# Optimization experiments

Measured on AMD Instinct MI355X. Metric: run time of the kernel, lower is better.

Reference implementation:

```python
import jax, jax.numpy as jnp
import numpy as np

B, N, D, M = 8, 8192, 256, 2  # M from init_kwargs


def setup_inputs() -> dict:
    key = jax.random.key(0)
    ks = jax.random.split(key, 10)
    g_names = ['G_l_ii', 'G_l_ij', 'G_l_ji', 'G_l_jj', 'G_u_ii', 'G_u_ij', 'G_u_ji', 'G_u_jj']
    inp = {'input': jax.random.normal(ks[0], (B, N, D), dtype=jnp.float32)}
    for i, name in enumerate(g_names):
        inp[name] = jax.random.normal(ks[1 + i], (B, N - 1), dtype=jnp.float32)
    inp['Diag'] = jax.random.normal(ks[9], (B, N), dtype=jnp.float32)
    inp['transform'] = 1
    return inp


def _banded_sweep(x, a0, b0, lo, dm, hi, aL, bL):
    # One tridiagonal Givens sweep over axis 1 of x [B,N,D].
    # row 0:       a0*x[0]   + b0*x[1]
    # rows 1..N-2: lo*x[i-1] + dm*x[i] + hi*x[i+1]
    # row N-1:     aL*x[N-2] + bL*x[N-1]
    n = x.shape[1]
    y0 = a0[:, None, None] * x[:, 0:1] + b0[:, None, None] * x[:, 1:2]
    ym = (lo[:, :, None] * x[:, :-2]
          + dm[:, :, None] * x[:, 1:n - 1]
          + hi[:, :, None] * x[:, 2:])
    yl = aL[:, None, None] * x[:, n - 2:n - 1] + bL[:, None, None] * x[:, n - 1:n]
    return jnp.concatenate([y0, ym, yl], axis=1)


def _forward(x, gl_ii, gl_ij, gl_ji, gl_jj, gu_ii, gu_ij, gu_ji, gu_jj, diag, transform):
    b, n, d = x.shape
    if transform:
        # stride permutation (only defined for even N in the original)
        x = x.reshape(b, n // M, M, d).transpose(0, 2, 1, 3).reshape(b, n, d)
    else:
        x = diag[:, :, None] * x
    # upper sweep -> Y
    y = _banded_sweep(
        x,
        gu_ii[:, 0], gu_ij[:, 0],
        gu_ji[:, :-1], gu_jj[:, :-1] * gu_ii[:, 1:], gu_jj[:, :-1] * gu_ij[:, 1:],
        gu_ji[:, n - 2], gu_jj[:, n - 2])
    # lower sweep -> Z
    z = _banded_sweep(
        y,
        gl_ii[:, 0], gl_ij[:, 0],
        gl_ii[:, 1:] * gl_ji[:, :-1], gl_ii[:, 1:] * gl_jj[:, :-1], gl_ij[:, 1:],
        gl_ji[:, n - 2], gl_jj[:, n - 2])
    if transform:
        z = diag[:, :, None] * z
    else:
        z = z.reshape(b, n // M, M, d).transpose(0, 2, 1, 3).reshape(b, n, d)
    return z


def reference(input, G_l_ii, G_l_ij, G_l_ji, G_l_jj, G_u_ii, G_u_ij, G_u_ji, G_u_jj, Diag, transform):
    return _forward(input, G_l_ii, G_l_ij, G_l_ji, G_l_jj,
                    G_u_ii, G_u_ij, G_u_ji, G_u_jj, Diag, transform)
```

## Files before the change

### kernel.cpp

```cpp
#include <hip/hip_runtime.h>

#define NN 8192
#define DD 256
#define NH (NN / 2)
#define BB 8
#define RPW 8
#define WPB 4
#define NBLK (BB * NN / RPW / WPB)
#define CPX (NBLK / 8)

typedef float fx4 __attribute__((ext_vector_type(4)));

__device__ __forceinline__ float4 gload4(const float* p) {
    fx4 t;
    asm volatile("global_load_dwordx4 %0, %1, off" : "=v"(t) : "v"(p) : "memory");
    return make_float4(t.x, t.y, t.z, t.w);
}

__device__ __forceinline__ float4 f4_scale(float s, float4 v) {
    return make_float4(s * v.x, s * v.y, s * v.z, s * v.w);
}
__device__ __forceinline__ float4 f4_fma(float s, float4 v, float4 a) {
    return make_float4(fmaf(s, v.x, a.x), fmaf(s, v.y, a.y),
                       fmaf(s, v.z, a.z), fmaf(s, v.w, a.w));
}

__global__ __launch_bounds__(256) void dhhp_kernel(
    const float* __restrict__ x,
    const float* __restrict__ gl_ii, const float* __restrict__ gl_ij,
    const float* __restrict__ gl_ji, const float* __restrict__ gl_jj,
    const float* __restrict__ gu_ii, const float* __restrict__ gu_ij,
    const float* __restrict__ gu_ji, const float* __restrict__ gu_jj,
    const float* __restrict__ diag, const int* __restrict__ transform,
    float* __restrict__ out)
{
    const int bid = blockIdx.x;
    const int swz = (bid & 7) * CPX + (bid >> 3);
    int wid = swz * WPB + (threadIdx.x >> 6);
    wid = __builtin_amdgcn_readfirstlane(wid);
    const int b   = wid >> 10;
    const int j0  = (wid & 1023) << 3;
    const int col = (threadIdx.x & 63) << 2;
    const int tr  = *transform;

    const float* xb  = x    + (size_t)b * NN * DD;
    const float* db  = diag + (size_t)b * NN;
    const float* uii = gu_ii + (size_t)b * (NN - 1);
    const float* uij = gu_ij + (size_t)b * (NN - 1);
    const float* uji = gu_ji + (size_t)b * (NN - 1);
    const float* ujj = gu_jj + (size_t)b * (NN - 1);
    const float* lii = gl_ii + (size_t)b * (NN - 1);
    const float* lij = gl_ij + (size_t)b * (NN - 1);
    const float* lji = gl_ji + (size_t)b * (NN - 1);
    const float* ljj = gl_jj + (size_t)b * (NN - 1);
    float* ob = out + (size_t)b * NN * DD;

    int ics[RPW + 4];
    const float* ap[RPW + 4];
    #pragma unroll
    for (int t = 0; t < RPW + 4; ++t) {
        int i  = j0 - 2 + t;
        int ic = i < 0 ? 0 : (i > NN - 1 ? NN - 1 : i);
        ics[t] = ic;
        int r  = tr ? ((ic < NH) ? (ic << 1) : (((ic - NH) << 1) | 1)) : ic;
        ap[t]  = xb + (size_t)r * DD + col;
    }
    float4 xr[RPW + 4];
    #pragma unroll
    for (int t = 0; t < RPW + 4; ++t) xr[t] = gload4(ap[t]);
    asm volatile("s_waitcnt vmcnt(0)" ::: "memory");

    if (!tr) {
        #pragma unroll
        for (int t = 0; t < RPW + 4; ++t) xr[t] = f4_scale(db[ics[t]], xr[t]);
    }

    auto yInner = [&](int i, float4 xm, float4 xc, float4 xp) -> float4 {
        float lo  = uji[i - 1];
        float cjj = ujj[i - 1];
        float dm  = cjj * uii[i];
        float hi  = cjj * uij[i];
        float4 r = f4_scale(lo, xm);
        r = f4_fma(dm, xc, r);
        r = f4_fma(hi, xp, r);
        return r;
    };
    auto yAny = [&](int i, float4 xm, float4 xc, float4 xp) -> float4 {
        int ic = i < 0 ? 0 : (i > NN - 1 ? NN - 1 : i);
        if (ic == 0)      return f4_fma(uii[0], xc, f4_scale(uij[0], xp));
        if (ic == NN - 1) return f4_fma(uji[NN - 2], xm, f4_scale(ujj[NN - 2], xc));
        return yInner(ic, xm, xc, xp);
    };
    auto zInner = [&](int j, float4 ym, float4 yc, float4 yp) -> float4 {
        float ci = lii[j];
        float lo = ci * lji[j - 1];
        float dm = ci * ljj[j - 1];
        float hi = lij[j];
        float4 r = f4_scale(lo, ym);
        r = f4_fma(dm, yc, r);
        r = f4_fma(hi, yp, r);
        return r;
    };
    auto zAny = [&](int j, float4 ym, float4 yc, float4 yp) -> float4 {
        if (j == 0)      return f4_fma(lii[0], yc, f4_scale(lij[0], yp));
        if (j == NN - 1) return f4_fma(lji[NN - 2], ym, f4_scale(ljj[NN - 2], yc));
        return zInner(j, ym, yc, yp);
    };
    auto storeRow = [&](int j, float4 z) {
        int jo;
        float4 o;
        if (tr) { o = f4_scale(db[j], z); jo = j; }
        else    { o = z; jo = (j & 1) ? (NH + (j >> 1)) : (j >> 1); }
        *reinterpret_cast<float4*>(ob + (size_t)jo * DD + col) = o;
    };

    float4 yr[RPW + 2];
    const bool interior = (j0 >= 2) && (j0 <= NN - RPW - 2);

    if (interior) {
        #pragma unroll
        for (int t = 0; t < RPW + 2; ++t)
            yr[t] = yInner(j0 - 1 + t, xr[t], xr[t + 1], xr[t + 2]);
        #pragma unroll
        for (int t = 0; t < RPW; ++t)
            storeRow(j0 + t, zInner(j0 + t, yr[t], yr[t + 1], yr[t + 2]));
    } else {
        #pragma unroll
        for (int t = 0; t < RPW + 2; ++t)
            yr[t] = yAny(j0 - 1 + t, xr[t], xr[t + 1], xr[t + 2]);
        #pragma unroll
        for (int t = 0; t < RPW; ++t)
            storeRow(j0 + t, zAny(j0 + t, yr[t], yr[t + 1], yr[t + 2]));
    }
}

extern "C" void kernel_launch(void* const* d_in, const int* in_sizes, int n_in,
                              void* d_out, int out_size, void* d_ws, size_t ws_size,
                              hipStream_t stream) {
    const float* x     = (const float*)d_in[0];
    const float* gl_ii = (const float*)d_in[1];
    const float* gl_ij = (const float*)d_in[2];
    const float* gl_ji = (const float*)d_in[3];
    const float* gl_jj = (const float*)d_in[4];
    const float* gu_ii = (const float*)d_in[5];
    const float* gu_ij = (const float*)d_in[6];
    const float* gu_ji = (const float*)d_in[7];
    const float* gu_jj = (const float*)d_in[8];
    const float* diag  = (const float*)d_in[9];
    const int* transform = (const int*)d_in[10];
    float* out = (float*)d_out;

    dim3 grid(NBLK);
    dim3 block(256);
    hipLaunchKernelGGL(dhhp_kernel, grid, block, 0, stream,
                       x, gl_ii, gl_ij, gl_ji, gl_jj,
                       gu_ii, gu_ij, gu_ji, gu_jj, diag, transform, out);
}
```

Before: 30.83 us.

## Process two row tiles per wave with staged vmcnt waits to overlap loads

Each wave now handles two 8-row tiles instead of one, so the grid is halved. All 24 row loads for both tiles are issued up front. Partial s_waitcnt vmcnt waits then let the first tile's compute and stores run while the second tile's loads are still in flight. This aims to raise memory-level parallelism per wave and hide load latency, at the cost of more registers and hand-counted vmcnt values that depend on the order loads and stores complete.

```diff
diff --git a/kernel.cpp b/kernel.cpp
--- a/kernel.cpp
+++ b/kernel.cpp
@@ -6,8 +6,11 @@
 #define BB 8
 #define RPW 8
 #define WPB 4
-#define NBLK (BB * NN / RPW / WPB)
+#define RPT (RPW * WPB)
+#define TPB 2
+#define NBLK (BB * NN / (RPT * TPB))
 #define CPX (NBLK / 8)
+#define WROWS (RPW + 4)
 
 typedef float fx4 __attribute__((ext_vector_type(4)));
 
@@ -36,10 +39,9 @@
 {
     const int bid = blockIdx.x;
     const int swz = (bid & 7) * CPX + (bid >> 3);
-    int wid = swz * WPB + (threadIdx.x >> 6);
-    wid = __builtin_amdgcn_readfirstlane(wid);
-    const int b   = wid >> 10;
-    const int j0  = (wid & 1023) << 3;
+    const int b   = __builtin_amdgcn_readfirstlane(swz >> 7);
+    const int t0  = __builtin_amdgcn_readfirstlane((swz & 127) << 6);
+    const int w   = __builtin_amdgcn_readfirstlane(threadIdx.x >> 6);
     const int col = (threadIdx.x & 63) << 2;
     const int tr  = *transform;
 
@@ -55,25 +57,31 @@
     const float* ljj = gl_jj + (size_t)b * (NN - 1);
     float* ob = out + (size_t)b * NN * DD;
 
-    int ics[RPW + 4];
-    const float* ap[RPW + 4];
+    const int j0a = t0 + (w << 3);
+    const int j0b = j0a + RPT;
+
+    int icsA[WROWS], icsB[WROWS];
+    const float* apA[WROWS];
+    const float* apB[WROWS];
     #pragma unroll
-    for (int t = 0; t < RPW + 4; ++t) {
-        int i  = j0 - 2 + t;
-        int ic = i < 0 ? 0 : (i > NN - 1 ? NN - 1 : i);
-        ics[t] = ic;
-        int r  = tr ? ((ic < NH) ? (ic << 1) : (((ic - NH) << 1) | 1)) : ic;
-        ap[t]  = xb + (size_t)r * DD + col;
+    for (int t = 0; t < WROWS; ++t) {
+        int ia  = j0a - 2 + t;
+        int ica = ia < 0 ? 0 : (ia > NN - 1 ? NN - 1 : ia);
+        icsA[t] = ica;
+        int ra  = tr ? ((ica < NH) ? (ica << 1) : (((ica - NH) << 1) | 1)) : ica;
+        apA[t]  = xb + (size_t)ra * DD + col;
+        int ib  = j0b - 2 + t;
+        int icb = ib < 0 ? 0 : (ib > NN - 1 ? NN - 1 : ib);
+        icsB[t] = icb;
+        int rb  = tr ? ((icb < NH) ? (icb << 1) : (((icb - NH) << 1) | 1)) : icb;
+        apB[t]  = xb + (size_t)rb * DD + col;
     }
-    float4 xr[RPW + 4];
+
+    float4 xrA[WROWS], xrB[WROWS];
     #pragma unroll
-    for (int t = 0; t < RPW + 4; ++t) xr[t] = gload4(ap[t]);
-    asm volatile("s_waitcnt vmcnt(0)" ::: "memory");
-
-    if (!tr) {
-        #pragma unroll
-        for (int t = 0; t < RPW + 4; ++t) xr[t] = f4_scale(db[ics[t]], xr[t]);
-    }
+    for (int t = 0; t < WROWS; ++t) xrA[t] = gload4(apA[t]);
+    #pragma unroll
+    for (int t = 0; t < WROWS; ++t) xrB[t] = gload4(apB[t]);
 
     auto yInner = [&](int i, float4 xm, float4 xc, float4 xp) -> float4 {
         float lo  = uji[i - 1];
@@ -113,25 +121,37 @@
         else    { o = z; jo = (j & 1) ? (NH + (j >> 1)) : (j >> 1); }
         *reinterpret_cast<float4*>(ob + (size_t)jo * DD + col) = o;
     };
+    auto computeTile = [&](int j0, float4 (&xr)[WROWS], int (&ics)[WROWS]) {
+        if (!tr) {
+            #pragma unroll
+            for (int t = 0; t < WROWS; ++t) xr[t] = f4_scale(db[ics[t]], xr[t]);
+        }
+        float4 yr[RPW + 2];
+        const bool interior = (j0 >= 2) && (j0 <= NN - RPW - 2);
+        if (interior) {
+            #pragma unroll
+            for (int t = 0; t < RPW + 2; ++t)
+                yr[t] = yInner(j0 - 1 + t, xr[t], xr[t + 1], xr[t + 2]);
+            #pragma unroll
+            for (int t = 0; t < RPW; ++t)
+                storeRow(j0 + t, zInner(j0 + t, yr[t], yr[t + 1], yr[t + 2]));
+        } else {
+            #pragma unroll
+            for (int t = 0; t < RPW + 2; ++t)
+                yr[t] = yAny(j0 - 1 + t, xr[t], xr[t + 1], xr[t + 2]);
+            #pragma unroll
+            for (int t = 0; t < RPW; ++t)
+                storeRow(j0 + t, zAny(j0 + t, yr[t], yr[t + 1], yr[t + 2]));
+        }
+    };
 
-    float4 yr[RPW + 2];
-    const bool interior = (j0 >= 2) && (j0 <= NN - RPW - 2);
+    asm volatile("s_waitcnt vmcnt(12)" ::: "memory");
+    __builtin_amdgcn_sched_barrier(0);
+    computeTile(j0a, xrA, icsA);
 
-    if (interior) {
-        #pragma unroll
-        for (int t = 0; t < RPW + 2; ++t)
-            yr[t] = yInner(j0 - 1 + t, xr[t], xr[t + 1], xr[t + 2]);
-        #pragma unroll
-        for (int t = 0; t < RPW; ++t)
-            storeRow(j0 + t, zInner(j0 + t, yr[t], yr[t + 1], yr[t + 2]));
-    } else {
-        #pragma unroll
-        for (int t = 0; t < RPW + 2; ++t)
-            yr[t] = yAny(j0 - 1 + t, xr[t], xr[t + 1], xr[t + 2]);
-        #pragma unroll
-        for (int t = 0; t < RPW; ++t)
-            storeRow(j0 + t, zAny(j0 + t, yr[t], yr[t + 1], yr[t + 2]));
-    }
+    asm volatile("s_waitcnt vmcnt(8)" ::: "memory");
+    __builtin_amdgcn_sched_barrier(0);
+    computeTile(j0b, xrB, icsB);
 }
 
 extern "C" void kernel_launch(void* const* d_in, const int* in_sizes, int n_in,
```

New measurement: 35.69 us. +15.7%, slower.
